# Kernel tuning notes

Hardware: AMD Instinct MI355X
Metric: run time of the kernel (lower is better)

## Reference

```python
import jax, jax.numpy as jnp
import numpy as np

B, S = 2048, 16384
DELAY = 5.0  # self._delay


def setup_inputs() -> dict:
    key = jax.random.key(0)
    k1, k2, k3 = jax.random.split(key, 3)
    logits = jax.random.normal(k1, (B, S, 1), dtype=jnp.float32)
    # ragged valid lengths; positions >= length are zero-padded (what the
    # torch while-loop trims as trailing zeros)
    lengths = jax.random.randint(k2, (B,), S // 4, S, dtype=jnp.int32)
    pad_mask = jnp.arange(S)[None, :] < lengths[:, None]  # [B,S]
    logits = logits * pad_mask[:, :, None].astype(jnp.float32)
    target = jax.random.uniform(k3, (B, 1), dtype=jnp.float32)
    return {"input": logits, "lengths": lengths, "target": target}


def reference(input, lengths, target):
    # input: [B,S,1] zero-padded logits; target: [B,1]
    x = input[..., 0]  # [B,S]
    seq = x.shape[1]
    # Replicate the torch trimming: last = -1; while pred[last]==0: last-=1;
    # pred = pred[:last] keeps exactly `idx` elements where idx is the index
    # of the last nonzero entry.
    nz = x != 0.0
    idx = seq - 1 - jnp.argmax(nz[:, ::-1], axis=1)  # [B], kept length L_i
    pos = jnp.arange(seq)
    keep = (pos[None, :] < idx[:, None]).astype(x.dtype)  # [B,S]
    # BCEWithLogits, reduction='none', default weights
    t = target  # [B,1] broadcasts over S
    bce = jnp.maximum(x, 0.0) - x * t + jnp.log1p(jnp.exp(-jnp.abs(x)))
    # position-dependent confidence weight: sigmoid(j - delay), masked to kept region
    w = jax.nn.sigmoid(pos.astype(x.dtype) - DELAY)[None, :] * keep  # [B,S]
    per_sample = (bce * w).sum(axis=1) / w.sum(axis=1)  # [B]
    return per_sample.mean()
```

## Files before the change

kernel.cpp:

```cpp
#include <hip/hip_runtime.h>
#include <math.h>


#define LN2F 0.69314718055994531f

__device__ __forceinline__ float bce_nat(float x, float t) {
    const float e = __expf(-fabsf(x));
    return fmaf(-x, t, fmaxf(x, 0.0f) + __logf(1.0f + e));
}

#define ACC(xv) do {                                   \
    const float e_ = __expf(-fabsf(xv));               \
    Alog += __log2f(1.0f + e_);                        \
    Alin += fmaf(-(xv), t, fmaxf((xv), 0.0f)); } while (0)

__global__ __launch_bounds__(256) void half_row_kernel(
    const float* __restrict__ x, const int* __restrict__ lengths,
    const float* __restrict__ target, float4* __restrict__ pA,
    float4* __restrict__ pB, int S)
{
    const int bid = blockIdx.x;
    const int b = bid >> 1;
    const bool isB = (bid & 1) != 0;
    const float* row = x + (size_t)b * (size_t)S;
    const float t = target[b];
    const int tid = threadIdx.x;
    const int len = min(max(lengths[b], 1), S);
    const int L4 = (len + 3) & ~3;
    const int H  = (L4 >> 3) << 2;
    const int lo = isB ? H : 0;
    const int hi = isB ? L4 : H;
    const int n  = hi - lo;
    const int lastb = lo + (((n - 1) >> 12) << 12);

    __shared__ float s_head[24];
    __shared__ float sLin[4], sLog[4], sV[4];
    __shared__ int   sI[4];
    __shared__ float s_lin, s_log;

    if (!isB && tid < 6)
        *reinterpret_cast<float4*>(&s_head[tid * 4]) =
            *reinterpret_cast<const float4*>(row + tid * 4);

    float Alin = 0.0f, Alog = 0.0f;
    int maxidx = -1; float mval = 0.0f;

    for (int base = lo; base < lastb; base += 4096) {
        const int j0 = base + tid * 4;
        const float4 v0 = *reinterpret_cast<const float4*>(row + j0);
        const float4 v1 = *reinterpret_cast<const float4*>(row + j0 + 1024);
        const float4 v2 = *reinterpret_cast<const float4*>(row + j0 + 2048);
        const float4 v3 = *reinterpret_cast<const float4*>(row + j0 + 3072);
        const float vs[16] = {v0.x, v0.y, v0.z, v0.w, v1.x, v1.y, v1.z, v1.w,
                              v2.x, v2.y, v2.z, v2.w, v3.x, v3.y, v3.z, v3.w};
        #pragma unroll
        for (int k = 0; k < 16; ++k) { const float xv = vs[k]; ACC(xv); }
    }

    if (isB) {
        #pragma unroll
        for (int seg = 0; seg < 4; ++seg) {
            const int j0 = lastb + (seg << 10) + tid * 4;
            if (j0 < hi) {
                const float4 v = *reinterpret_cast<const float4*>(row + j0);
                const float vs[4] = {v.x, v.y, v.z, v.w};
                #pragma unroll
                for (int k = 0; k < 4; ++k) {
                    const float xv = vs[k]; ACC(xv);
                    if (xv != 0.0f) { maxidx = j0 + k; mval = xv; }
                }
            }
        }
    } else {
        #pragma unroll
        for (int seg = 0; seg < 4; ++seg) {
            const int j0 = lastb + (seg << 10) + tid * 4;
            if (j0 < hi) {
                const float4 v = *reinterpret_cast<const float4*>(row + j0);
                const float vs[4] = {v.x, v.y, v.z, v.w};
                #pragma unroll
                for (int k = 0; k < 4; ++k) { const float xv = vs[k]; ACC(xv); }
            }
        }
    }

    #pragma unroll
    for (int off = 32; off > 0; off >>= 1) {
        Alin += __shfl_down(Alin, off);
        Alog += __shfl_down(Alog, off);
        const int   oi = __shfl_down(maxidx, off);
        const float ov = __shfl_down(mval, off);
        if (oi > maxidx) { maxidx = oi; mval = ov; }
    }
    const int wave = tid >> 6;
    if ((tid & 63) == 0) { sLin[wave] = Alin; sLog[wave] = Alog;
                           sI[wave] = maxidx; sV[wave] = mval; }
    __syncthreads();

    if (isB) {
        if (tid == 0) {
            #pragma unroll
            for (int w = 1; w < 4; ++w) {
                Alin += sLin[w]; Alog += sLog[w];
                if (sI[w] > maxidx) { maxidx = sI[w]; mval = sV[w]; }
            }
            int idx; float mv;
            if (maxidx < 0) { idx = hi - 1; mv = 0.0f; }
            else            { idx = maxidx; mv = mval; }
            const float e_m  = __expf(-fabsf(mv));
            const float logC = Alog - __log2f(1.0f + e_m)
                               - (float)(L4 - 1 - idx);
            const float linC = Alin - fmaf(-mv, t, fmaxf(mv, 0.0f));
            pB[b] = make_float4(linC, logC, (float)(idx - 22), 0.0f);
        }
    } else {
        if (tid == 0) {
            #pragma unroll
            for (int w = 1; w < 4; ++w) { Alin += sLin[w]; Alog += sLog[w]; }
            s_lin = Alin; s_log = Alog;
        }
        __syncthreads();
        if (tid < 64) {
            float c = 0.0f, d = 0.0f;
            if (tid < 22) {
                const float sg = 1.0f / (1.0f + __expf(5.0f - (float)tid));
                c = bce_nat(s_head[tid], t) * (sg - 1.0f);
                d = sg;
            }
            #pragma unroll
            for (int off = 32; off > 0; off >>= 1) {
                c += __shfl_down(c, off);
                d += __shfl_down(d, off);
            }
            if (tid == 0)
                pA[b] = make_float4(s_lin + c, s_log, d, 0.0f);
        }
    }
}

__device__ __forceinline__ float finish_row(float4 a, float4 bq) {
    return (a.x + bq.x + LN2F * (a.y + bq.y)) / (a.z + bq.z);
}

__global__ __launch_bounds__(1024) void combine_kernel(
    const float4* __restrict__ pA, const float4* __restrict__ pB,
    float* __restrict__ out, int B)
{
    const int tid = threadIdx.x;
    float s = 0.0f;
    for (int r0 = tid; r0 < B; r0 += 2048) {
        const int r1 = r0 + 1024;
        const bool h1 = r1 < B;
        const float4 a0 = pA[r0], b0 = pB[r0];
        float4 a1, b1;
        if (h1) { a1 = pA[r1]; b1 = pB[r1]; }
        s += finish_row(a0, b0);
        if (h1) s += finish_row(a1, b1);
    }
    #pragma unroll
    for (int off = 32; off > 0; off >>= 1) s += __shfl_down(s, off);
    __shared__ float sw[16];
    if ((tid & 63) == 0) sw[tid >> 6] = s;
    __syncthreads();
    if (tid == 0) {
        float tot = 0.0f;
        #pragma unroll
        for (int w = 0; w < 16; ++w) tot += sw[w];
        out[0] = tot / (float)B;
    }
}

extern "C" void kernel_launch(void* const* d_in, const int* in_sizes, int n_in,
                              void* d_out, int out_size, void* d_ws, size_t ws_size,
                              hipStream_t stream) {
    const float* logits  = (const float*)d_in[0];
    const int*   lengths = (const int*)d_in[1];
    const float* target  = (const float*)d_in[2];
    float* out = (float*)d_out;

    const int B = in_sizes[2];
    const int S = in_sizes[0] / B;

    float4* pA = (float4*)d_ws;
    float4* pB = pA + B;

    half_row_kernel<<<2 * B, 256, 0, stream>>>(logits, lengths, target,
                                               pA, pB, S);
    combine_kernel<<<1, 1024, 0, stream>>>(pA, pB, out, B);
}
```

Baseline: 23.25 us.

## Fully unroll half-row loads and replace per-element log with product of terms

Result: faster. 22.54 us (-3.1%).

```diff
diff --git a/kernel.cpp b/kernel.cpp
--- a/kernel.cpp
+++ b/kernel.cpp
@@ -8,11 +8,6 @@
     const float e = __expf(-fabsf(x));
     return fmaf(-x, t, fmaxf(x, 0.0f) + __logf(1.0f + e));
 }
-
-#define ACC(xv) do {                                   \
-    const float e_ = __expf(-fabsf(xv));               \
-    Alog += __log2f(1.0f + e_);                        \
-    Alin += fmaf(-(xv), t, fmaxf((xv), 0.0f)); } while (0)
 
 __global__ __launch_bounds__(256) void half_row_kernel(
     const float* __restrict__ x, const int* __restrict__ lengths,
@@ -30,8 +25,6 @@
     const int H  = (L4 >> 3) << 2;
     const int lo = isB ? H : 0;
     const int hi = isB ? L4 : H;
-    const int n  = hi - lo;
-    const int lastb = lo + (((n - 1) >> 12) << 12);
 
     __shared__ float s_head[24];
     __shared__ float sLin[4], sLog[4], sV[4];
@@ -42,47 +35,55 @@
         *reinterpret_cast<float4*>(&s_head[tid * 4]) =
             *reinterpret_cast<const float4*>(row + tid * 4);
 
-    float Alin = 0.0f, Alog = 0.0f;
+    const int j0 = lo + tid * 4;
+
+    float4 v0, v1, v2, v3, v4, v5, v6, v7;
+    const bool g0 = (j0          ) < hi;
+    const bool g1 = (j0 + 1 * 1024) < hi;
+    const bool g2 = (j0 + 2 * 1024) < hi;
+    const bool g3 = (j0 + 3 * 1024) < hi;
+    const bool g4 = (j0 + 4 * 1024) < hi;
+    const bool g5 = (j0 + 5 * 1024) < hi;
+    const bool g6 = (j0 + 6 * 1024) < hi;
+    const bool g7 = (j0 + 7 * 1024) < hi;
+    v0 = *reinterpret_cast<const float4*>(row + j0);
+    v1 = *reinterpret_cast<const float4*>(row + j0 + 1 * 1024);
+    if (g2) v2 = *reinterpret_cast<const float4*>(row + j0 + 2 * 1024);
+    if (g3) v3 = *reinterpret_cast<const float4*>(row + j0 + 3 * 1024);
+    if (g4) v4 = *reinterpret_cast<const float4*>(row + j0 + 4 * 1024);
+    if (g5) v5 = *reinterpret_cast<const float4*>(row + j0 + 5 * 1024);
+    if (g6) v6 = *reinterpret_cast<const float4*>(row + j0 + 6 * 1024);
+    if (g7) v7 = *reinterpret_cast<const float4*>(row + j0 + 7 * 1024);
+
+    float P0 = 1.0f, P1 = 1.0f;
+    float A0 = 0.0f, A1 = 0.0f;
     int maxidx = -1; float mval = 0.0f;
 
-    for (int base = lo; base < lastb; base += 4096) {
-        const int j0 = base + tid * 4;
-        const float4 v0 = *reinterpret_cast<const float4*>(row + j0);
-        const float4 v1 = *reinterpret_cast<const float4*>(row + j0 + 1024);
-        const float4 v2 = *reinterpret_cast<const float4*>(row + j0 + 2048);
-        const float4 v3 = *reinterpret_cast<const float4*>(row + j0 + 3072);
-        const float vs[16] = {v0.x, v0.y, v0.z, v0.w, v1.x, v1.y, v1.z, v1.w,
-                              v2.x, v2.y, v2.z, v2.w, v3.x, v3.y, v3.z, v3.w};
-        #pragma unroll
-        for (int k = 0; k < 16; ++k) { const float xv = vs[k]; ACC(xv); }
-    }
+#define SEG(vv, gg, ss, PP, AA) do {                                   \
+    if (gg) {                                                          \
+        const float s_[4] = {vv.x, vv.y, vv.z, vv.w};                  \
+        const int jb_ = j0 + (ss) * 1024;                              \
+        _Pragma("unroll")                                              \
+        for (int k_ = 0; k_ < 4; ++k_) {                               \
+            const float xv_ = s_[k_];                                  \
+            PP *= 1.0f + __expf(-fabsf(xv_));                          \
+            AA += fmaf(-xv_, t, fmaxf(xv_, 0.0f));                     \
+            if (xv_ != 0.0f) { maxidx = jb_ + k_; mval = xv_; }        \
+        }                                                              \
+    } } while (0)
 
-    if (isB) {
-        #pragma unroll
-        for (int seg = 0; seg < 4; ++seg) {
-            const int j0 = lastb + (seg << 10) + tid * 4;
-            if (j0 < hi) {
-                const float4 v = *reinterpret_cast<const float4*>(row + j0);
-                const float vs[4] = {v.x, v.y, v.z, v.w};
-                #pragma unroll
-                for (int k = 0; k < 4; ++k) {
-                    const float xv = vs[k]; ACC(xv);
-                    if (xv != 0.0f) { maxidx = j0 + k; mval = xv; }
-                }
-            }
-        }
-    } else {
-        #pragma unroll
-        for (int seg = 0; seg < 4; ++seg) {
-            const int j0 = lastb + (seg << 10) + tid * 4;
-            if (j0 < hi) {
-                const float4 v = *reinterpret_cast<const float4*>(row + j0);
-                const float vs[4] = {v.x, v.y, v.z, v.w};
-                #pragma unroll
-                for (int k = 0; k < 4; ++k) { const float xv = vs[k]; ACC(xv); }
-            }
-        }
-    }
+    SEG(v0, g0, 0, P0, A0);
+    SEG(v1, g1, 1, P1, A1);
+    SEG(v2, g2, 2, P0, A0);
+    SEG(v3, g3, 3, P1, A1);
+    SEG(v4, g4, 4, P0, A0);
+    SEG(v5, g5, 5, P1, A1);
+    SEG(v6, g6, 6, P0, A0);
+    SEG(v7, g7, 7, P1, A1);
+#undef SEG
+
+    float Alin = A0 + A1;
+    float Alog = __log2f(P0 * P1);
 
     #pragma unroll
     for (int off = 32; off > 0; off >>= 1) {
```
